# Kernel tuning notes

Measured on AMD Instinct MI355X. Metric: run time of the kernel, lower is better.

The kernel has to match this reference:

```python
import jax, jax.numpy as jnp
import numpy as np

B, CW_DIM = 256, 8192
DIM_EMBED = 128
DICT_SIZE = 4096
DIM_CODES = CW_DIM // DIM_EMBED  # 64


def setup_inputs() -> dict:
    key = jax.random.key(0)
    k1, k2 = jax.random.split(key)
    x = jax.random.normal(k1, (B, CW_DIM), dtype=jnp.float32)
    dictionary = jax.random.normal(k2, (DIM_CODES, DICT_SIZE, DIM_EMBED), dtype=jnp.float32)
    return {"x": x, "dictionary": dictionary}


def reference(x, dictionary):
    """VQVAE.quantise (eval mode): pairwise sq-distance -> argmin -> gather + one-hot.

    x: [B, cw_dim], dictionary: [C, S, E] with cw_dim = C*E.
    Returns (cw_embed [B, C*E], one_hot_idx [B, C, S]).
    """
    Bb, D = x.shape
    C, S, E = dictionary.shape
    xr = x.reshape(Bb, C, E)                                   # [B, C, E]
    x_sq = jnp.sum(xr * xr, axis=-1, keepdims=True)            # [B, C, 1]
    d_sq = jnp.sum(dictionary * dictionary, axis=-1)           # [C, S]
    cross = jnp.einsum('bce,cse->bcs', xr, dictionary)         # [B, C, S] (GEMM)
    dist = x_sq + d_sq[None, :, :] - 2.0 * cross               # [B, C, S]
    idx = jnp.argmin(dist, axis=-1)                            # [B, C]
    # gather nearest codes: dictionary[c, idx[b,c]] -> [B, C, E]
    code_ids = jnp.arange(C)[None, :]                          # [1, C]
    cw_embed = dictionary[code_ids, idx]                       # [B, C, E]
    cw_embed = cw_embed.reshape(Bb, C * E)                     # [B, cw_dim]
    one_hot_idx = jax.nn.one_hot(idx, S, dtype=x.dtype)        # [B, C, S]
    return cw_embed, one_hot_idx
```

## Files before the change

### kernel.cpp

```cpp
#include <hip/hip_runtime.h>
#include <stdint.h>


#define B_SZ 256
#define C_SZ 64
#define E_SZ 128
#define S_SZ 4096
#define CW   8192
#define LDB  136

typedef __attribute__((ext_vector_type(4))) float    float4a;
typedef __attribute__((ext_vector_type(8))) _Float16 half8;

__device__ __forceinline__ void split8(float4a f0, float4a f1, half8& hi, half8& lo) {
    #pragma unroll
    for (int j = 0; j < 4; ++j) {
        _Float16 h0 = (_Float16)f0[j];
        hi[j]     = h0;
        lo[j]     = (_Float16)(f0[j] - (float)h0);
        _Float16 h1 = (_Float16)f1[j];
        hi[4 + j] = h1;
        lo[4 + j] = (_Float16)(f1[j] - (float)h1);
    }
}

__global__ __launch_bounds__(512, 2) void argmin_mfma(
    const float* __restrict__ x,
    const float* __restrict__ dict,
    float* __restrict__ cw_out,
    float* __restrict__ oh)
{
    __shared__ __attribute__((aligned(16))) _Float16 bh[2][128 * LDB];
    __shared__ __attribute__((aligned(16))) _Float16 bl[2][128 * LDB];
    __shared__ float4a dsqp[2][128];
    __shared__ int     fid[64];
    float* rv = reinterpret_cast<float*>(bh);
    int*   ri = reinterpret_cast<int*>(bl);

    const int tid   = threadIdx.x;
    const int lane  = tid & 63;
    const int quad  = lane >> 4;
    const int l15   = lane & 15;
    const int wid   = tid >> 6;
    const int mhalf = wid & 1;
    const int nquad = wid >> 1;
    const int c     = blockIdx.x & 63;
    const int btile = blockIdx.x >> 6;

    int m_attr[4], n_attr[4];
    {
        half8 ones, enc;
        #pragma unroll
        for (int j = 0; j < 8; ++j) { ones[j] = (_Float16)1.0f; enc[j] = (_Float16)(float)l15; }
        float4a z = {0.f, 0.f, 0.f, 0.f};
        float4a pr = __builtin_amdgcn_mfma_f32_16x16x32_f16(enc, ones, z, 0, 0, 0);
        float4a pc = __builtin_amdgcn_mfma_f32_16x16x32_f16(ones, enc, z, 0, 0, 0);
        #pragma unroll
        for (int r = 0; r < 4; ++r) {
            m_attr[r] = (int)(pr[r] * 0.03125f + 0.5f);
            n_attr[r] = (int)(pc[r] * 0.03125f + 0.5f);
        }
    }

    half8 ah[2][4], al[2][4];
    #pragma unroll
    for (int mi = 0; mi < 2; ++mi) {
        int b = btile * 64 + mhalf * 32 + mi * 16 + l15;
        const float* xr = x + (size_t)b * CW + c * E_SZ;
        #pragma unroll
        for (int kk = 0; kk < 4; ++kk) {
            float4a f0 = *reinterpret_cast<const float4a*>(xr + kk * 32 + quad * 8);
            float4a f1 = *reinterpret_cast<const float4a*>(xr + kk * 32 + quad * 8 + 4);
            split8(f0, f1, ah[mi][kk], al[mi][kk]);
        }
    }

    const int srow = tid >> 2;
    const int kq   = (tid & 3) * 32;
    const int q4   = tid & 3;
    const float* drow = dict + ((size_t)c * S_SZ + srow) * E_SZ + kq;

    float* ohb = oh + ((size_t)(btile * 64) * C_SZ + c) * S_SZ;
    const size_t oh_bstride = (size_t)C_SZ * S_SZ;

    float4a pf0[4], pf1[4];
    #pragma unroll
    for (int ck = 0; ck < 4; ++ck) {
        pf0[ck] = *reinterpret_cast<const float4a*>(drow + ck * 8);
        pf1[ck] = *reinterpret_cast<const float4a*>(drow + ck * 8 + 4);
    }
    {
        float dp = 0.f;
        #pragma unroll
        for (int ck = 0; ck < 4; ++ck) {
            half8 h, l;
            split8(pf0[ck], pf1[ck], h, l);
            #pragma unroll
            for (int j = 0; j < 4; ++j) {
                dp = fmaf(pf0[ck][j], pf0[ck][j], dp);
                dp = fmaf(pf1[ck][j], pf1[ck][j], dp);
            }
            *reinterpret_cast<half8*>(&bh[0][srow * LDB + kq + ck * 8]) = h;
            *reinterpret_cast<half8*>(&bl[0][srow * LDB + kq + ck * 8]) = l;
        }
        dsqp[0][srow][q4] = dp;
    }

    float bestv[8];
    int   besti[8];
    #pragma unroll
    for (int i = 0; i < 8; ++i) { bestv[i] = 3.4e38f; besti[i] = 0; }

    __syncthreads();

    int cur = 0;
    for (int it = 0; it < 32; ++it) {
        const int s0 = it * 128;

        if (it + 1 < 32) {
            const float* dr = drow + (size_t)(it + 1) * (128 * E_SZ);
            #pragma unroll
            for (int ck = 0; ck < 4; ++ck) {
                pf0[ck] = *reinterpret_cast<const float4a*>(dr + ck * 8);
                pf1[ck] = *reinterpret_cast<const float4a*>(dr + ck * 8 + 4);
            }
        }

        {
            float4a zz = {0.f, 0.f, 0.f, 0.f};
            float* z0 = ohb + (size_t)(it * 2) * oh_bstride;
            float* z1 = z0 + oh_bstride;
            __builtin_nontemporal_store(zz, reinterpret_cast<float4a*>(z0) + tid);
            __builtin_nontemporal_store(zz, reinterpret_cast<float4a*>(z0) + 512 + tid);
            __builtin_nontemporal_store(zz, reinterpret_cast<float4a*>(z1) + tid);
            __builtin_nontemporal_store(zz, reinterpret_cast<float4a*>(z1) + 512 + tid);
        }

        const _Float16* bhc = bh[cur];
        const _Float16* blc = bl[cur];
        float4a acc[2][2] = {{{0.f,0.f,0.f,0.f},{0.f,0.f,0.f,0.f}},
                             {{0.f,0.f,0.f,0.f},{0.f,0.f,0.f,0.f}}};
        __builtin_amdgcn_s_setprio(1);
        #pragma unroll
        for (int kk = 0; kk < 4; ++kk) {
            half8 bhf[2], blf[2];
            #pragma unroll
            for (int ni = 0; ni < 2; ++ni) {
                const int sl = nquad * 32 + ni * 16 + l15;
                bhf[ni] = *reinterpret_cast<const half8*>(bhc + sl * LDB + kk * 32 + quad * 8);
                blf[ni] = *reinterpret_cast<const half8*>(blc + sl * LDB + kk * 32 + quad * 8);
            }
            #pragma unroll
            for (int mi = 0; mi < 2; ++mi)
                #pragma unroll
                for (int ni = 0; ni < 2; ++ni) {
                    acc[mi][ni] = __builtin_amdgcn_mfma_f32_16x16x32_f16(
                        ah[mi][kk], bhf[ni], acc[mi][ni], 0, 0, 0);
                    acc[mi][ni] = __builtin_amdgcn_mfma_f32_16x16x32_f16(
                        ah[mi][kk], blf[ni], acc[mi][ni], 0, 0, 0);
                    acc[mi][ni] = __builtin_amdgcn_mfma_f32_16x16x32_f16(
                        al[mi][kk], bhf[ni], acc[mi][ni], 0, 0, 0);
                }
        }
        __builtin_amdgcn_s_setprio(0);

        #pragma unroll
        for (int ni = 0; ni < 2; ++ni)
            #pragma unroll
            for (int r = 0; r < 4; ++r) {
                const int sl = nquad * 32 + ni * 16 + n_attr[r];
                float4a q4v = dsqp[cur][sl];
                float dsq = (q4v[0] + q4v[1]) + (q4v[2] + q4v[3]);
                int sg = s0 + sl;
                #pragma unroll
                for (int mi = 0; mi < 2; ++mi) {
                    float dist = dsq - 2.0f * acc[mi][ni][r];
                    int slot = mi * 4 + r;
                    if (dist < bestv[slot]) { bestv[slot] = dist; besti[slot] = sg; }
                }
            }

        if (it + 1 < 32) {
            const int nb = cur ^ 1;
            float dp = 0.f;
            #pragma unroll
            for (int ck = 0; ck < 4; ++ck) {
                half8 h, l;
                split8(pf0[ck], pf1[ck], h, l);
                #pragma unroll
                for (int j = 0; j < 4; ++j) {
                    dp = fmaf(pf0[ck][j], pf0[ck][j], dp);
                    dp = fmaf(pf1[ck][j], pf1[ck][j], dp);
                }
                *reinterpret_cast<half8*>(&bh[nb][srow * LDB + kq + ck * 8]) = h;
                *reinterpret_cast<half8*>(&bl[nb][srow * LDB + kq + ck * 8]) = l;
            }
            dsqp[nb][srow][q4] = dp;
        }
        __syncthreads();
        cur ^= 1;
    }


    #pragma unroll
    for (int mi = 0; mi < 2; ++mi)
        #pragma unroll
        for (int r = 0; r < 4; ++r) {
            int row = mhalf * 32 + mi * 16 + m_attr[r];
            int col = nquad * 16 + n_attr[r];
            rv[row * 64 + col] = bestv[mi * 4 + r];
            ri[row * 64 + col] = besti[mi * 4 + r];
        }
    __syncthreads();

    if (tid < 64) {
        float bv = 3.4e38f; int bi = 0x7fffffff;
        for (int j = 0; j < 64; ++j) {
            float v = rv[tid * 64 + j];
            int   i = ri[tid * 64 + j];
            if (v < bv || (v == bv && i < bi)) { bv = v; bi = i; }
        }
        fid[tid] = bi;
        ohb[(size_t)tid * oh_bstride + bi] = 1.0f;
    }
    __syncthreads();

    for (int u = tid; u < 64 * 32; u += 512) {
        int row = u >> 5, ch = u & 31;
        int bi = fid[row];
        float4a v = *reinterpret_cast<const float4a*>(
            dict + ((size_t)c * S_SZ + bi) * E_SZ + ch * 4);
        *reinterpret_cast<float4a*>(
            cw_out + (size_t)(btile * 64 + row) * CW + c * E_SZ + ch * 4) = v;
    }
}

extern "C" void kernel_launch(void* const* d_in, const int* in_sizes, int n_in,
                              void* d_out, int out_size, void* d_ws, size_t ws_size,
                              hipStream_t stream) {
    const float* x    = (const float*)d_in[0];
    const float* dict = (const float*)d_in[1];
    float* out = (float*)d_out;
    float* oh  = out + (size_t)B_SZ * CW;

    argmin_mfma<<<dim3(256), dim3(512), 0, stream>>>(x, dict, out, oh);
}
```

Measured before the change: 462.5 us.

## Split codebook search across two blocks and merge argmin in a finalize kernel

```diff
diff --git a/kernel.cpp b/kernel.cpp
--- a/kernel.cpp
+++ b/kernel.cpp
@@ -7,6 +7,7 @@
 #define E_SZ 128
 #define S_SZ 4096
 #define CW   8192
+#define TS   64
 #define LDB  136
 
 typedef __attribute__((ext_vector_type(4))) float    float4a;
@@ -24,16 +25,15 @@
     }
 }
 
-__global__ __launch_bounds__(512, 2) void argmin_mfma(
+__global__ __launch_bounds__(512, 4) void argmin_mfma(
     const float* __restrict__ x,
     const float* __restrict__ dict,
     float* __restrict__ cw_out,
     float* __restrict__ oh)
 {
-    __shared__ __attribute__((aligned(16))) _Float16 bh[2][128 * LDB];
-    __shared__ __attribute__((aligned(16))) _Float16 bl[2][128 * LDB];
-    __shared__ float4a dsqp[2][128];
-    __shared__ int     fid[64];
+    __shared__ __attribute__((aligned(16))) _Float16 bh[2][TS * LDB];
+    __shared__ __attribute__((aligned(16))) _Float16 bl[2][TS * LDB];
+    __shared__ float dsqp[2][TS][8];
     float* rv = reinterpret_cast<float*>(bh);
     int*   ri = reinterpret_cast<int*>(bl);
 
@@ -45,7 +45,9 @@
     const int mhalf = wid & 1;
     const int nquad = wid >> 1;
     const int c     = blockIdx.x & 63;
-    const int btile = blockIdx.x >> 6;
+    const int btile = (blockIdx.x >> 6) & 3;
+    const int shalf = blockIdx.x >> 8;
+    const int sbase = shalf * 2048;
 
     int m_attr[4], n_attr[4];
     {
@@ -75,35 +77,32 @@
         }
     }
 
-    const int srow = tid >> 2;
-    const int kq   = (tid & 3) * 32;
-    const int q4   = tid & 3;
-    const float* drow = dict + ((size_t)c * S_SZ + srow) * E_SZ + kq;
-
-    float* ohb = oh + ((size_t)(btile * 64) * C_SZ + c) * S_SZ;
+    const int srow = tid >> 3;
+    const int kq   = (tid & 7) * 16;
+    const float* drow = dict + ((size_t)c * S_SZ + sbase + srow) * E_SZ + kq;
+
+    float* ohb = oh + ((size_t)(btile * 64) * C_SZ + c) * S_SZ + sbase;
     const size_t oh_bstride = (size_t)C_SZ * S_SZ;
 
-    float4a pf0[4], pf1[4];
-    #pragma unroll
-    for (int ck = 0; ck < 4; ++ck) {
-        pf0[ck] = *reinterpret_cast<const float4a*>(drow + ck * 8);
-        pf1[ck] = *reinterpret_cast<const float4a*>(drow + ck * 8 + 4);
-    }
+    float4a pf[4];
+    #pragma unroll
+    for (int ck = 0; ck < 4; ++ck)
+        pf[ck] = *reinterpret_cast<const float4a*>(drow + ck * 4);
     {
         float dp = 0.f;
         #pragma unroll
-        for (int ck = 0; ck < 4; ++ck) {
+        for (int ck = 0; ck < 2; ++ck) {
             half8 h, l;
-            split8(pf0[ck], pf1[ck], h, l);
+            split8(pf[2 * ck], pf[2 * ck + 1], h, l);
             #pragma unroll
             for (int j = 0; j < 4; ++j) {
-                dp = fmaf(pf0[ck][j], pf0[ck][j], dp);
-                dp = fmaf(pf1[ck][j], pf1[ck][j], dp);
+                dp = fmaf(pf[2 * ck][j], pf[2 * ck][j], dp);
+                dp = fmaf(pf[2 * ck + 1][j], pf[2 * ck + 1][j], dp);
             }
             *reinterpret_cast<half8*>(&bh[0][srow * LDB + kq + ck * 8]) = h;
             *reinterpret_cast<half8*>(&bl[0][srow * LDB + kq + ck * 8]) = l;
         }
-        dsqp[0][srow][q4] = dp;
+        dsqp[0][srow][tid & 7] = dp;
     }
 
     float bestv[8];
@@ -115,15 +114,11 @@
 
     int cur = 0;
     for (int it = 0; it < 32; ++it) {
-        const int s0 = it * 128;
-
         if (it + 1 < 32) {
-            const float* dr = drow + (size_t)(it + 1) * (128 * E_SZ);
-            #pragma unroll
-            for (int ck = 0; ck < 4; ++ck) {
-                pf0[ck] = *reinterpret_cast<const float4a*>(dr + ck * 8);
-                pf1[ck] = *reinterpret_cast<const float4a*>(dr + ck * 8 + 4);
-            }
+            const float* dr = drow + (size_t)(it + 1) * (TS * E_SZ);
+            #pragma unroll
+            for (int ck = 0; ck < 4; ++ck)
+                pf[ck] = *reinterpret_cast<const float4a*>(dr + ck * 4);
         }
 
         {
@@ -131,71 +126,62 @@
             float* z0 = ohb + (size_t)(it * 2) * oh_bstride;
             float* z1 = z0 + oh_bstride;
             __builtin_nontemporal_store(zz, reinterpret_cast<float4a*>(z0) + tid);
-            __builtin_nontemporal_store(zz, reinterpret_cast<float4a*>(z0) + 512 + tid);
             __builtin_nontemporal_store(zz, reinterpret_cast<float4a*>(z1) + tid);
-            __builtin_nontemporal_store(zz, reinterpret_cast<float4a*>(z1) + 512 + tid);
         }
 
         const _Float16* bhc = bh[cur];
         const _Float16* blc = bl[cur];
-        float4a acc[2][2] = {{{0.f,0.f,0.f,0.f},{0.f,0.f,0.f,0.f}},
-                             {{0.f,0.f,0.f,0.f},{0.f,0.f,0.f,0.f}}};
+        float4a acc[2] = {{0.f,0.f,0.f,0.f},{0.f,0.f,0.f,0.f}};
         __builtin_amdgcn_s_setprio(1);
         #pragma unroll
         for (int kk = 0; kk < 4; ++kk) {
-            half8 bhf[2], blf[2];
-            #pragma unroll
-            for (int ni = 0; ni < 2; ++ni) {
-                const int sl = nquad * 32 + ni * 16 + l15;
-                bhf[ni] = *reinterpret_cast<const half8*>(bhc + sl * LDB + kk * 32 + quad * 8);
-                blf[ni] = *reinterpret_cast<const half8*>(blc + sl * LDB + kk * 32 + quad * 8);
-            }
-            #pragma unroll
-            for (int mi = 0; mi < 2; ++mi)
-                #pragma unroll
-                for (int ni = 0; ni < 2; ++ni) {
-                    acc[mi][ni] = __builtin_amdgcn_mfma_f32_16x16x32_f16(
-                        ah[mi][kk], bhf[ni], acc[mi][ni], 0, 0, 0);
-                    acc[mi][ni] = __builtin_amdgcn_mfma_f32_16x16x32_f16(
-                        ah[mi][kk], blf[ni], acc[mi][ni], 0, 0, 0);
-                    acc[mi][ni] = __builtin_amdgcn_mfma_f32_16x16x32_f16(
-                        al[mi][kk], bhf[ni], acc[mi][ni], 0, 0, 0);
-                }
+            const int sl = nquad * 16 + l15;
+            half8 bhf = *reinterpret_cast<const half8*>(bhc + sl * LDB + kk * 32 + quad * 8);
+            half8 blf = *reinterpret_cast<const half8*>(blc + sl * LDB + kk * 32 + quad * 8);
+            #pragma unroll
+            for (int mi = 0; mi < 2; ++mi) {
+                acc[mi] = __builtin_amdgcn_mfma_f32_16x16x32_f16(
+                    ah[mi][kk], bhf, acc[mi], 0, 0, 0);
+                acc[mi] = __builtin_amdgcn_mfma_f32_16x16x32_f16(
+                    ah[mi][kk], blf, acc[mi], 0, 0, 0);
+                acc[mi] = __builtin_amdgcn_mfma_f32_16x16x32_f16(
+                    al[mi][kk], bhf, acc[mi], 0, 0, 0);
+            }
         }
         __builtin_amdgcn_s_setprio(0);
 
         #pragma unroll
-        for (int ni = 0; ni < 2; ++ni)
-            #pragma unroll
-            for (int r = 0; r < 4; ++r) {
-                const int sl = nquad * 32 + ni * 16 + n_attr[r];
-                float4a q4v = dsqp[cur][sl];
-                float dsq = (q4v[0] + q4v[1]) + (q4v[2] + q4v[3]);
-                int sg = s0 + sl;
-                #pragma unroll
-                for (int mi = 0; mi < 2; ++mi) {
-                    float dist = dsq - 2.0f * acc[mi][ni][r];
-                    int slot = mi * 4 + r;
-                    if (dist < bestv[slot]) { bestv[slot] = dist; besti[slot] = sg; }
-                }
-            }
+        for (int r = 0; r < 4; ++r) {
+            const int sl = nquad * 16 + n_attr[r];
+            float4a qa = *reinterpret_cast<const float4a*>(&dsqp[cur][sl][0]);
+            float4a qb = *reinterpret_cast<const float4a*>(&dsqp[cur][sl][4]);
+            float dsq = ((qa[0] + qa[1]) + (qa[2] + qa[3]))
+                      + ((qb[0] + qb[1]) + (qb[2] + qb[3]));
+            int sg = sbase + it * TS + sl;
+            #pragma unroll
+            for (int mi = 0; mi < 2; ++mi) {
+                float dist = dsq - 2.0f * acc[mi][r];
+                int slot = mi * 4 + r;
+                if (dist < bestv[slot]) { bestv[slot] = dist; besti[slot] = sg; }
+            }
+        }
 
         if (it + 1 < 32) {
             const int nb = cur ^ 1;
             float dp = 0.f;
             #pragma unroll
-            for (int ck = 0; ck < 4; ++ck) {
+            for (int ck = 0; ck < 2; ++ck) {
                 half8 h, l;
-                split8(pf0[ck], pf1[ck], h, l);
+                split8(pf[2 * ck], pf[2 * ck + 1], h, l);
                 #pragma unroll
                 for (int j = 0; j < 4; ++j) {
-                    dp = fmaf(pf0[ck][j], pf0[ck][j], dp);
-                    dp = fmaf(pf1[ck][j], pf1[ck][j], dp);
+                    dp = fmaf(pf[2 * ck][j], pf[2 * ck][j], dp);
+                    dp = fmaf(pf[2 * ck + 1][j], pf[2 * ck + 1][j], dp);
                 }
                 *reinterpret_cast<half8*>(&bh[nb][srow * LDB + kq + ck * 8]) = h;
                 *reinterpret_cast<half8*>(&bl[nb][srow * LDB + kq + ck * 8]) = l;
             }
-            dsqp[nb][srow][q4] = dp;
+            dsqp[nb][srow][tid & 7] = dp;
         }
         __syncthreads();
         cur ^= 1;
@@ -220,19 +206,40 @@
             int   i = ri[tid * 64 + j];
             if (v < bv || (v == bv && i < bi)) { bv = v; bi = i; }
         }
+        float* cp = cw_out + (size_t)(btile * 64 + tid) * CW + c * E_SZ + shalf * 2;
+        cp[0] = bv;
+        cp[1] = __int_as_float(bi);
+    }
+}
+
+__global__ __launch_bounds__(256) void finalize(
+    const float* __restrict__ dict,
+    float* __restrict__ cw_out,
+    float* __restrict__ oh)
+{
+    __shared__ int fid[64];
+    const int c     = blockIdx.x & 63;
+    const int btile = blockIdx.x >> 6;
+    const int tid   = threadIdx.x;
+
+    if (tid < 64) {
+        const float* cp = cw_out + (size_t)(btile * 64 + tid) * CW + c * E_SZ;
+        float d0 = cp[0]; int i0 = __float_as_int(cp[1]);
+        float d1 = cp[2]; int i1 = __float_as_int(cp[3]);
+        int bi = (d1 < d0) ? i1 : i0;
         fid[tid] = bi;
-        ohb[(size_t)tid * oh_bstride + bi] = 1.0f;
+        oh[((size_t)(btile * 64 + tid) * C_SZ + c) * S_SZ + bi] = 1.0f;
     }
     __syncthreads();
 
-    for (int u = tid; u < 64 * 32; u += 512) {
-        int row = u >> 5, ch = u & 31;
-        int bi = fid[row];
-        float4a v = *reinterpret_cast<const float4a*>(
-            dict + ((size_t)c * S_SZ + bi) * E_SZ + ch * 4);
-        *reinterpret_cast<float4a*>(
-            cw_out + (size_t)(btile * 64 + row) * CW + c * E_SZ + ch * 4) = v;
-    }
+    const int row = tid >> 2, q = tid & 3;
+    const int bi = fid[row];
+    const float4a* src = reinterpret_cast<const float4a*>(
+        dict + ((size_t)c * S_SZ + bi) * E_SZ) + q * 8;
+    float4a* dst = reinterpret_cast<float4a*>(
+        cw_out + (size_t)(btile * 64 + row) * CW + c * E_SZ) + q * 8;
+    #pragma unroll
+    for (int j = 0; j < 8; ++j) dst[j] = src[j];
 }
 
 extern "C" void kernel_launch(void* const* d_in, const int* in_sizes, int n_in,
@@ -243,5 +250,6 @@
     float* out = (float*)d_out;
     float* oh  = out + (size_t)B_SZ * CW;
 
-    argmin_mfma<<<dim3(256), dim3(512), 0, stream>>>(x, dict, out, oh);
-}
+    argmin_mfma<<<dim3(512), dim3(512), 0, stream>>>(x, dict, out, oh);
+    finalize<<<dim3(256), dim3(256), 0, stream>>>(dict, out, oh);
+}
```

Result: slower. 500.3 us (+8.2%).
